# Kernel optimization log

Hardware: AMD Instinct MI355X
Metric: run time of the kernel (lower is better)

The kernel has to match this reference:

```python
import jax, jax.numpy as jnp
import numpy as np

INPUT_DIM = 1024
BOTTLENECK = 256
NUM_Q = 8
CODEBOOK = 1024
COMMIT_W = 0.25

def setup_inputs() -> dict:
    key = jax.random.key(0)
    ks = jax.random.split(key, 10)
    s_in = 1.0 / np.sqrt(INPUT_DIM)
    s_bn = 1.0 / np.sqrt(BOTTLENECK)
    return {
        'x': jax.random.normal(ks[0], (8, 2048, INPUT_DIM), jnp.float32),
        'W_e1': jax.random.uniform(ks[1], (INPUT_DIM, INPUT_DIM), jnp.float32, -s_in, s_in),
        'b_e1': jnp.zeros((INPUT_DIM,), jnp.float32),
        'W_e2': jax.random.uniform(ks[2], (INPUT_DIM, BOTTLENECK), jnp.float32, -s_in, s_in),
        'b_e2': jnp.zeros((BOTTLENECK,), jnp.float32),
        'codebooks': jax.random.normal(ks[3], (NUM_Q, CODEBOOK, BOTTLENECK), jnp.float32),
        'W_d1': jax.random.uniform(ks[4], (BOTTLENECK, INPUT_DIM), jnp.float32, -s_bn, s_bn),
        'b_d1': jnp.zeros((INPUT_DIM,), jnp.float32),
        'W_d2': jax.random.uniform(ks[5], (INPUT_DIM, INPUT_DIM), jnp.float32, -s_in, s_in),
        'b_d2': jnp.zeros((INPUT_DIM,), jnp.float32),
    }

def _gelu(x):
    return jax.nn.gelu(x, approximate=False)  # torch nn.GELU default = exact erf

def _rvq(z_flat, codebooks):
    # z_flat: [N, D]; codebooks: [Q, K, D]
    def step(res, cb):
        # squared L2 distances via expansion: [N, K]
        d2 = (jnp.sum(res * res, -1, keepdims=True)
              - 2.0 * res @ cb.T
              + jnp.sum(cb * cb, -1))
        idx = jnp.argmin(d2, axis=-1)                      # [N]
        q = jax.lax.stop_gradient(jnp.take(cb, idx, 0))    # [N, D] (EMA codebook: no grad)
        closs = jnp.mean((res - q) ** 2)
        return res - q, (idx, q, closs)
    _, (indices, qs, closses) = jax.lax.scan(step, z_flat, codebooks)
    q_total = jnp.sum(qs, axis=0)
    # straight-through estimator
    quantized = z_flat + jax.lax.stop_gradient(q_total - z_flat)
    commitment = COMMIT_W * jnp.mean(closses)
    return quantized, indices, commitment

def reference(x, W_e1, b_e1, W_e2, b_e2, codebooks, W_d1, b_d1, W_d2, b_d2):
    lead = x.shape[:-1]
    z = _gelu(x @ W_e1 + b_e1) @ W_e2 + b_e2               # [..., BOTTLENECK]
    zf = z.reshape(-1, BOTTLENECK)
    qf, indices, commitment = _rvq(zf, codebooks)
    quantized = qf.reshape(*lead, BOTTLENECK)
    indices = indices.reshape(NUM_Q, *lead)
    reconstructed = _gelu(quantized @ W_d1 + b_d1) @ W_d2 + b_d2
    return z, quantized, indices, reconstructed, commitment
```

## Files before the change

kernel.cpp:

```cpp
#include <hip/hip_runtime.h>
#include <math.h>

#define NROWS 16384
#define DIN   1024
#define DBN   256
#define NQ    8
#define NCODE 1024
#define MARGIN 2.0f

#define OFF_Z    0
#define OFF_Q    4194304
#define OFF_IDX  8388608
#define OFF_REC  8519680
#define OFF_COM  25296896

typedef __attribute__((ext_vector_type(8))) short short8v;
typedef __attribute__((ext_vector_type(4))) float f32x4;

__device__ __forceinline__ float gelu_f(float x) {
  return 0.5f * x * (1.0f + erff(x * 0.70710678118654752440f));
}

__device__ __forceinline__ ushort f2b(float x) {
  unsigned u = __float_as_uint(x);
  unsigned r = u + 0x7FFF + ((u >> 16) & 1);
  return (ushort)(r >> 16);
}
__device__ __forceinline__ float b2f(ushort u) {
  return __uint_as_float((unsigned)u << 16);
}
__device__ __forceinline__ void split3(float v, ushort& s1, ushort& s2, ushort& s3) {
  s1 = f2b(v);
  const float r1 = v - b2f(s1);
  s2 = f2b(r1);
  const float r2 = r1 - b2f(s2);
  s3 = f2b(r2);
}

template<bool GELU, int NB, int OUT>
__global__ __launch_bounds__(256) void gemm6(
    const float* __restrict__ Af,
    const ushort* __restrict__ B1, const ushort* __restrict__ B2,
    const ushort* __restrict__ B3,
    const float* __restrict__ bias,
    float* __restrict__ C0, float* __restrict__ C1,
    int N, int K)
{
  constexpr int BN = NB * 32;
  __shared__ char lds[24576 + BN * 192];
  char* ldsA = lds;
  char* ldsB = lds + 24576;
  const int tid = threadIdx.x;
  const int bm = blockIdx.x * 128;
  const int bn = blockIdx.y * BN;
  const int lane = tid & 63;
  const int wid = tid >> 6;
  const int wr = wid >> 1, wc = wid & 1;

  const int srow = tid >> 1, skh = tid & 1;
  const float* Ap = Af + (size_t)(bm + srow) * K + skh * 16;
  const int abase = srow * 192;
  const int aswz = (srow & 7) << 4;

  f32x4 acc[4][NB];
  #pragma unroll
  for (int m = 0; m < 4; ++m)
    #pragma unroll
    for (int n = 0; n < NB; ++n) acc[m][n] = (f32x4)0.f;

  union U8 { ushort u[8]; short8v v; };

  const int nt = K >> 5;
  for (int t = 0; t < nt; ++t) {
    const int k0 = t << 5;
    __syncthreads();
    float av[16];
    *(float4*)&av[0]  = *(const float4*)(Ap + k0);
    *(float4*)&av[4]  = *(const float4*)(Ap + k0 + 4);
    *(float4*)&av[8]  = *(const float4*)(Ap + k0 + 8);
    *(float4*)&av[12] = *(const float4*)(Ap + k0 + 12);
    U8 p1[2], p2[2], p3[2];
    #pragma unroll
    for (int i = 0; i < 16; ++i) {
      ushort s1, s2, s3;
      split3(av[i], s1, s2, s3);
      p1[i >> 3].u[i & 7] = s1;
      p2[i >> 3].u[i & 7] = s2;
      p3[i >> 3].u[i & 7] = s3;
    }
    #pragma unroll
    for (int h2 = 0; h2 < 2; ++h2) {
      const int kb = skh * 32 + h2 * 16;
      *(short8v*)(ldsA + ((abase + 0   + kb) ^ aswz)) = p1[h2].v;
      *(short8v*)(ldsA + ((abase + 64  + kb) ^ aswz)) = p2[h2].v;
      *(short8v*)(ldsA + ((abase + 128 + kb) ^ aswz)) = p3[h2].v;
    }
    if (NB == 4) {
      const int br = tid >> 1, bk = tid & 1;
      const size_t g = (size_t)(bn + br) * K + k0 + bk * 16;
      const int bb = br * 192, bswz = (br & 7) << 4;
      #pragma unroll
      for (int h2 = 0; h2 < 2; ++h2) {
        const int kb = bk * 32 + h2 * 16;
        *(uint4*)(ldsB + ((bb + 0   + kb) ^ bswz)) = *(const uint4*)(B1 + g + h2 * 8);
        *(uint4*)(ldsB + ((bb + 64  + kb) ^ bswz)) = *(const uint4*)(B2 + g + h2 * 8);
        *(uint4*)(ldsB + ((bb + 128 + kb) ^ bswz)) = *(const uint4*)(B3 + g + h2 * 8);
      }
    } else {
      const int br = tid >> 2, bk = tid & 3;
      const size_t g = (size_t)(bn + br) * K + k0 + bk * 8;
      const int bb = br * 192, bswz = (br & 7) << 4;
      const int kb = bk * 16;
      *(uint4*)(ldsB + ((bb + 0   + kb) ^ bswz)) = *(const uint4*)(B1 + g);
      *(uint4*)(ldsB + ((bb + 64  + kb) ^ bswz)) = *(const uint4*)(B2 + g);
      *(uint4*)(ldsB + ((bb + 128 + kb) ^ bswz)) = *(const uint4*)(B3 + g);
    }
    __syncthreads();

    const int kq = (lane >> 4) << 4;
    short8v a1[4], a2[4], a3[4], b1v[NB], b2v[NB], b3v[NB];
    #pragma unroll
    for (int m = 0; m < 4; ++m) {
      const int row = wr * 64 + m * 16 + (lane & 15);
      const int base = row * 192, swz = (row & 7) << 4;
      a1[m] = *(const short8v*)(ldsA + ((base + 0   + kq) ^ swz));
      a2[m] = *(const short8v*)(ldsA + ((base + 64  + kq) ^ swz));
      a3[m] = *(const short8v*)(ldsA + ((base + 128 + kq) ^ swz));
    }
    #pragma unroll
    for (int n = 0; n < NB; ++n) {
      const int row = wc * (NB * 16) + n * 16 + (lane & 15);
      const int base = row * 192, swz = (row & 7) << 4;
      b1v[n] = *(const short8v*)(ldsB + ((base + 0   + kq) ^ swz));
      b2v[n] = *(const short8v*)(ldsB + ((base + 64  + kq) ^ swz));
      b3v[n] = *(const short8v*)(ldsB + ((base + 128 + kq) ^ swz));
    }
    #pragma unroll
    for (int m = 0; m < 4; ++m)
      #pragma unroll
      for (int n = 0; n < NB; ++n) {
        f32x4 a = acc[m][n];
        a = __builtin_amdgcn_mfma_f32_16x16x32_bf16(a3[m], b1v[n], a, 0, 0, 0);
        a = __builtin_amdgcn_mfma_f32_16x16x32_bf16(a1[m], b3v[n], a, 0, 0, 0);
        a = __builtin_amdgcn_mfma_f32_16x16x32_bf16(a2[m], b2v[n], a, 0, 0, 0);
        a = __builtin_amdgcn_mfma_f32_16x16x32_bf16(a2[m], b1v[n], a, 0, 0, 0);
        a = __builtin_amdgcn_mfma_f32_16x16x32_bf16(a1[m], b2v[n], a, 0, 0, 0);
        a = __builtin_amdgcn_mfma_f32_16x16x32_bf16(a1[m], b1v[n], a, 0, 0, 0);
        acc[m][n] = a;
      }
  }

  #pragma unroll
  for (int n = 0; n < NB; ++n) {
    const int col = bn + wc * (NB * 16) + n * 16 + (lane & 15);
    const float bb = bias[col];
    #pragma unroll
    for (int m = 0; m < 4; ++m) {
      const int row0 = bm + wr * 64 + m * 16 + ((lane >> 4) << 2);
      #pragma unroll
      for (int r = 0; r < 4; ++r) {
        float v = acc[m][n][r] + bb;
        if (GELU) v = gelu_f(v);
        C0[(size_t)(row0 + r) * N + col] = v;
        if (OUT == 1) C1[(size_t)(row0 + r) * N + col] = v;
      }
    }
  }
}

__device__ __forceinline__ void mm_core(
    const ushort* __restrict__ A, const ushort* __restrict__ B,
    int K, int bm, int bn, char* lds, f32x4 acc[4][4])
{
  char* ldsA = lds;
  char* ldsB = lds + 16384;
  const int tid = threadIdx.x;
  const int lane = tid & 63;
  const int wid = tid >> 6;
  const int wr = wid >> 1, wc = wid & 1;

  #pragma unroll
  for (int m = 0; m < 4; ++m)
    #pragma unroll
    for (int n = 0; n < 4; ++n) acc[m][n] = (f32x4)0.f;

  const int nt = K >> 6;
  for (int t = 0; t < nt; ++t) {
    const int k0 = t << 6;
    __syncthreads();
    #pragma unroll
    for (int c = 0; c < 4; ++c) {
      const int id = c * 256 + tid;
      const int row = id >> 3, k8 = id & 7;
      const uint4 va = *(const uint4*)(A + (size_t)(bm + row) * K + k0 + k8 * 8);
      const uint4 vb = *(const uint4*)(B + (size_t)(bn + row) * K + k0 + k8 * 8);
      const int off = (row * 128 + k8 * 16) ^ ((row & 7) << 4);
      *(uint4*)(ldsA + off) = va;
      *(uint4*)(ldsB + off) = vb;
    }
    __syncthreads();
    #pragma unroll
    for (int kk = 0; kk < 2; ++kk) {
      short8v af[4], bfr[4];
      #pragma unroll
      for (int m = 0; m < 4; ++m) {
        const int row = wr * 64 + m * 16 + (lane & 15);
        af[m] = *(const short8v*)(ldsA +
            ((row * 128 + kk * 64 + ((lane >> 4) << 4)) ^ ((row & 7) << 4)));
      }
      #pragma unroll
      for (int n = 0; n < 4; ++n) {
        const int row = wc * 64 + n * 16 + (lane & 15);
        bfr[n] = *(const short8v*)(ldsB +
            ((row * 128 + kk * 64 + ((lane >> 4) << 4)) ^ ((row & 7) << 4)));
      }
      #pragma unroll
      for (int m = 0; m < 4; ++m)
        #pragma unroll
        for (int n = 0; n < 4; ++n)
          acc[m][n] = __builtin_amdgcn_mfma_f32_16x16x32_bf16(
              af[m], bfr[n], acc[m][n], 0, 0, 0);
    }
  }
}

__global__ __launch_bounds__(256) void rvq_screen(
    const ushort* __restrict__ resb, const ushort* __restrict__ cbb,
    const float* __restrict__ cnorm, _Float16* __restrict__ D)
{
  __shared__ char lds[32768];
  f32x4 acc[4][4];
  const int bm = blockIdx.x * 128, bn = blockIdx.y * 128;
  mm_core(resb, cbb, DBN, bm, bn, lds, acc);
  const int lane = threadIdx.x & 63;
  const int wid = threadIdx.x >> 6;
  const int wr = wid >> 1, wc = wid & 1;
  #pragma unroll
  for (int n = 0; n < 4; ++n) {
    const int col = bn + wc * 64 + n * 16 + (lane & 15);
    const float cn = cnorm[col];
    #pragma unroll
    for (int m = 0; m < 4; ++m) {
      const int row0 = bm + wr * 64 + m * 16 + ((lane >> 4) << 2);
      #pragma unroll
      for (int r = 0; r < 4; ++r)
        D[(size_t)(row0 + r) * NCODE + col] = (_Float16)(cn - 2.0f * acc[m][n][r]);
    }
  }
}

template<bool GELU, bool OUTF>
__global__ __launch_bounds__(256) void gemm_bf16(
    const ushort* __restrict__ A, const ushort* __restrict__ Bt,
    const float* __restrict__ bias, float* __restrict__ Cf,
    ushort* __restrict__ Cb, int N, int K)
{
  __shared__ char lds[32768];
  f32x4 acc[4][4];
  const int bm = blockIdx.x * 128, bn = blockIdx.y * 128;
  mm_core(A, Bt, K, bm, bn, lds, acc);
  const int lane = threadIdx.x & 63;
  const int wid = threadIdx.x >> 6;
  const int wr = wid >> 1, wc = wid & 1;
  #pragma unroll
  for (int n = 0; n < 4; ++n) {
    const int col = bn + wc * 64 + n * 16 + (lane & 15);
    const float bb = bias[col];
    #pragma unroll
    for (int m = 0; m < 4; ++m) {
      const int row0 = bm + wr * 64 + m * 16 + ((lane >> 4) << 2);
      #pragma unroll
      for (int r = 0; r < 4; ++r) {
        float v = acc[m][n][r] + bb;
        if (GELU) v = gelu_f(v);
        if (OUTF) Cf[(size_t)(row0 + r) * N + col] = v;
        else      Cb[(size_t)(row0 + r) * N + col] = f2b(v);
      }
    }
  }
}

__global__ __launch_bounds__(256) void cnorm_kernel(
    const float* __restrict__ cb, float* __restrict__ cnorm)
{
  const int code = blockIdx.x * 4 + (threadIdx.x >> 6);
  const int lane = threadIdx.x & 63;
  float4 v = *(const float4*)(cb + (size_t)code * DBN + lane * 4);
  float s = v.x * v.x + v.y * v.y + v.z * v.z + v.w * v.w;
  #pragma unroll
  for (int o = 32; o > 0; o >>= 1) s += __shfl_down(s, o, 64);
  if (lane == 0) cnorm[code] = s;
}

__global__ __launch_bounds__(256) void rvq_rescore(
    const _Float16* __restrict__ D, const float* __restrict__ cb_s,
    const float* __restrict__ cnorm_s,
    float* __restrict__ res, ushort* __restrict__ resb,
    float* __restrict__ idx_out, float* __restrict__ closs_part)
{
  __shared__ int cnt[4];
  __shared__ ushort cand[4][128];
  __shared__ float wsum[4];
  const int w = threadIdx.x >> 6, lane = threadIdx.x & 63;
  const int row = blockIdx.x * 4 + w;
  if (lane == 0) cnt[w] = 0;

  union H8 { uint4 u; _Float16 h[8]; };
  const _Float16* Dr = D + (size_t)row * NCODE + lane * 16;
  H8 a0, a1;
  a0.u = *(const uint4*)(Dr);
  a1.u = *(const uint4*)(Dr + 8);
  float dv[16];
  #pragma unroll
  for (int i = 0; i < 8; ++i) { dv[i] = (float)a0.h[i]; dv[8 + i] = (float)a1.h[i]; }

  float mn = dv[0];
  #pragma unroll
  for (int i = 1; i < 16; ++i) mn = fminf(mn, dv[i]);
  #pragma unroll
  for (int o = 32; o > 0; o >>= 1) mn = fminf(mn, __shfl_xor(mn, o, 64));
  const float thr = mn + MARGIN;

  #pragma unroll
  for (int i = 0; i < 16; ++i)
    if (dv[i] < thr) {
      int p = atomicAdd(&cnt[w], 1);
      if (p < 128) cand[w][p] = (ushort)(lane * 16 + i);
    }
  const int ncand = min(cnt[w], 128);

  const float4 r4 = *(const float4*)(res + (size_t)row * DBN + lane * 4);
  float bestv = INFINITY; int besti = 0x7fffffff;
  for (int c = 0; c < ncand; ++c) {
    const int code = cand[w][c];
    const float4 c4 = *(const float4*)(cb_s + (size_t)code * DBN + lane * 4);
    float d = r4.x * c4.x + r4.y * c4.y + r4.z * c4.z + r4.w * c4.w;
    #pragma unroll
    for (int o = 32; o > 0; o >>= 1) d += __shfl_xor(d, o, 64);
    const float ex = cnorm_s[code] - 2.0f * d;
    if (ex < bestv || (ex == bestv && code < besti)) { bestv = ex; besti = code; }
  }

  const float4 q4 = *(const float4*)(cb_s + (size_t)besti * DBN + lane * 4);
  float4 n4;
  n4.x = r4.x - q4.x; n4.y = r4.y - q4.y; n4.z = r4.z - q4.z; n4.w = r4.w - q4.w;
  *(float4*)(res + (size_t)row * DBN + lane * 4) = n4;
  ushort4 nb;
  nb.x = f2b(n4.x); nb.y = f2b(n4.y); nb.z = f2b(n4.z); nb.w = f2b(n4.w);
  *(ushort4*)(resb + (size_t)row * DBN + lane * 4) = nb;

  float s = n4.x * n4.x + n4.y * n4.y + n4.z * n4.z + n4.w * n4.w;
  #pragma unroll
  for (int o = 32; o > 0; o >>= 1) s += __shfl_xor(s, o, 64);
  if (lane == 0) { wsum[w] = s; idx_out[row] = (float)besti; }
  __syncthreads();
  if (threadIdx.x == 0)
    closs_part[blockIdx.x] = wsum[0] + wsum[1] + wsum[2] + wsum[3];
}

__global__ __launch_bounds__(256) void qfix_gather(
    const float* __restrict__ z, const float* __restrict__ idxf,
    const float* __restrict__ cb, float* __restrict__ q, ushort* __restrict__ qb)
{
  const int w = threadIdx.x >> 6, lane = threadIdx.x & 63;
  const int row = blockIdx.x * 4 + w;
  float4 a; a.x = 0.f; a.y = 0.f; a.z = 0.f; a.w = 0.f;
  #pragma unroll
  for (int s = 0; s < NQ; ++s) {
    const int ix = (int)idxf[(size_t)s * NROWS + row];
    const float4 c4 = *(const float4*)(cb + ((size_t)s * NCODE + ix) * DBN + lane * 4);
    a.x += c4.x; a.y += c4.y; a.z += c4.z; a.w += c4.w;
  }
  const float4 z4 = *(const float4*)(z + (size_t)row * DBN + lane * 4);
  float4 qv;
  qv.x = z4.x + (a.x - z4.x); qv.y = z4.y + (a.y - z4.y);
  qv.z = z4.z + (a.z - z4.z); qv.w = z4.w + (a.w - z4.w);
  *(float4*)(q + (size_t)row * DBN + lane * 4) = qv;
  ushort4 qb4;
  qb4.x = f2b(qv.x); qb4.y = f2b(qv.y); qb4.z = f2b(qv.z); qb4.w = f2b(qv.w);
  *(ushort4*)(qb + (size_t)row * DBN + lane * 4) = qb4;
}

__global__ __launch_bounds__(256) void conv_flat(
    const float* __restrict__ in, ushort* __restrict__ out, int n4)
{
  const int i = blockIdx.x * 256 + threadIdx.x;
  if (i >= n4) return;
  const float4 v = *(const float4*)(in + (size_t)i * 4);
  ushort4 o;
  o.x = f2b(v.x); o.y = f2b(v.y); o.z = f2b(v.z); o.w = f2b(v.w);
  *(ushort4*)(out + (size_t)i * 4) = o;
}

__global__ __launch_bounds__(256) void convT(
    const float* __restrict__ in, ushort* __restrict__ out, int K, int N)
{
  __shared__ float t[32][33];
  const int k0 = blockIdx.x * 32, n0 = blockIdx.y * 32;
  const int tx = threadIdx.x & 31, ty = threadIdx.x >> 5;
  #pragma unroll
  for (int i = 0; i < 32; i += 8)
    t[ty + i][tx] = in[(size_t)(k0 + ty + i) * N + n0 + tx];
  __syncthreads();
  #pragma unroll
  for (int i = 0; i < 32; i += 8)
    out[(size_t)(n0 + ty + i) * K + k0 + tx] = f2b(t[tx][ty + i]);
}

__global__ __launch_bounds__(256) void convT_split3(
    const float* __restrict__ in, ushort* __restrict__ o1,
    ushort* __restrict__ o2, ushort* __restrict__ o3, int K, int N)
{
  __shared__ float t[32][33];
  const int k0 = blockIdx.x * 32, n0 = blockIdx.y * 32;
  const int tx = threadIdx.x & 31, ty = threadIdx.x >> 5;
  #pragma unroll
  for (int i = 0; i < 32; i += 8)
    t[ty + i][tx] = in[(size_t)(k0 + ty + i) * N + n0 + tx];
  __syncthreads();
  #pragma unroll
  for (int i = 0; i < 32; i += 8) {
    const float v = t[tx][ty + i];
    ushort s1, s2, s3;
    split3(v, s1, s2, s3);
    const size_t o = (size_t)(n0 + ty + i) * K + k0 + tx;
    o1[o] = s1; o2[o] = s2; o3[o] = s3;
  }
}

__global__ __launch_bounds__(256) void commit_kernel(
    const float* __restrict__ parts, float* __restrict__ out)
{
  __shared__ float sm[256];
  float s = 0.f;
  for (int i = threadIdx.x; i < NQ * 4096; i += 256) s += parts[i];
  sm[threadIdx.x] = s;
  __syncthreads();
  for (int st = 128; st > 0; st >>= 1) {
    if (threadIdx.x < st) sm[threadIdx.x] += sm[threadIdx.x + st];
    __syncthreads();
  }
  if (threadIdx.x == 0)
    out[0] = 0.25f * sm[0] / (8.0f * 4194304.0f);
}

extern "C" void kernel_launch(void* const* d_in, const int* in_sizes, int n_in,
                              void* d_out, int out_size, void* d_ws, size_t ws_size,
                              hipStream_t stream) {
  (void)in_sizes; (void)n_in; (void)out_size; (void)ws_size;
  const float* x    = (const float*)d_in[0];
  const float* W_e1 = (const float*)d_in[1];
  const float* b_e1 = (const float*)d_in[2];
  const float* W_e2 = (const float*)d_in[3];
  const float* b_e2 = (const float*)d_in[4];
  const float* cb   = (const float*)d_in[5];
  const float* W_d1 = (const float*)d_in[6];
  const float* b_d1 = (const float*)d_in[7];
  const float* W_d2 = (const float*)d_in[8];
  const float* b_d2 = (const float*)d_in[9];

  float* out = (float*)d_out;
  float* z_out   = out + OFF_Z;
  float* q_out   = out + OFF_Q;
  float* idx_out = out + OFF_IDX;
  float* rec_out = out + OFF_REC;
  float* com_out = out + OFF_COM;

  float* ws      = (float*)d_ws;
  float* hidden  = ws;
  float* res     = ws + 16777216;
  float* cnorm   = ws + 20971520;
  float* closs   = ws + 20979712;
  ushort* wtail  = (ushort*)(ws + 21012480);
  ushort* We2T1  = wtail;
  ushort* We2T2  = wtail + 262144;
  ushort* We2T3  = wtail + 524288;
  ushort* Wd1T   = wtail + 786432;
  ushort* Wd2T   = wtail + 1048576;

  ushort* resu   = (ushort*)res;
  ushort* We1T1  = resu;
  ushort* We1T2  = resu + 1048576;
  ushort* We1T3  = resu + 2097152;

  ushort* hregion = (ushort*)d_ws;
  _Float16* Dmat = (_Float16*)hregion;
  ushort* resb   = hregion + 16777216;
  ushort* cbb    = hregion + 20971520;
  ushort* qb     = hregion + 20971520;
  ushort* hidb   = hregion;

  cnorm_kernel<<<2048, 256, 0, stream>>>(cb, cnorm);
  convT_split3<<<dim3(32, 32), 256, 0, stream>>>(W_e1, We1T1, We1T2, We1T3, DIN, DIN);
  convT_split3<<<dim3(32, 8),  256, 0, stream>>>(W_e2, We2T1, We2T2, We2T3, DIN, DBN);
  convT<<<dim3(8, 32),  256, 0, stream>>>(W_d1, Wd1T, DBN, DIN);
  convT<<<dim3(32, 32), 256, 0, stream>>>(W_d2, Wd2T, DIN, DIN);

  gemm6<true,  4, 0><<<dim3(128, 8), 256, 0, stream>>>(
      x, We1T1, We1T2, We1T3, b_e1, hidden, nullptr, DIN, DIN);
  gemm6<false, 2, 1><<<dim3(128, 4), 256, 0, stream>>>(
      hidden, We2T1, We2T2, We2T3, b_e2, z_out, res, DBN, DIN);

  conv_flat<<<4096, 256, 0, stream>>>(res, resb, 1048576);
  conv_flat<<<2048, 256, 0, stream>>>(cb, cbb, 524288);

  for (int s = 0; s < NQ; ++s) {
    rvq_screen<<<dim3(128, 8), 256, 0, stream>>>(
        resb, cbb + (size_t)s * NCODE * DBN, cnorm + s * NCODE, Dmat);
    rvq_rescore<<<4096, 256, 0, stream>>>(
        Dmat, cb + (size_t)s * NCODE * DBN, cnorm + s * NCODE,
        res, resb, idx_out + (size_t)s * NROWS, closs + s * 4096);
  }

  qfix_gather<<<4096, 256, 0, stream>>>(z_out, idx_out, cb, q_out, qb);

  gemm_bf16<true,  false><<<dim3(128, 8), 256, 0, stream>>>(qb, Wd1T, b_d1, nullptr, hidb, DIN, DBN);
  gemm_bf16<false, true ><<<dim3(128, 8), 256, 0, stream>>>(hidb, Wd2T, b_d2, rec_out, nullptr, DIN, DIN);

  commit_kernel<<<1, 256, 0, stream>>>(closs, com_out);
}
```

Baseline: 682.1 us.

## Replace dense fp16 RVQ distance matrix with compact per-tile candidate records

```diff
diff --git a/kernel.cpp b/kernel.cpp
--- a/kernel.cpp
+++ b/kernel.cpp
@@ -226,26 +226,79 @@
 
 __global__ __launch_bounds__(256) void rvq_screen(
     const ushort* __restrict__ resb, const ushort* __restrict__ cbb,
-    const float* __restrict__ cnorm, _Float16* __restrict__ D)
+    const float* __restrict__ cnorm, uint4* __restrict__ Srec)
 {
   __shared__ char lds[32768];
   f32x4 acc[4][4];
   const int bm = blockIdx.x * 128, bn = blockIdx.y * 128;
   mm_core(resb, cbb, DBN, bm, bn, lds, acc);
-  const int lane = threadIdx.x & 63;
-  const int wid = threadIdx.x >> 6;
+  __syncthreads();
+
+  float* rv    = (float*)lds;
+  float* cminA = (float*)(lds + 16384);
+  int*   scnt  = (int*)(lds + 16896);
+  uint*  scand = (uint*)(lds + 17408);
+
+  const int tid = threadIdx.x;
+  const int lane = tid & 63;
+  const int wid = tid >> 6;
   const int wr = wid >> 1, wc = wid & 1;
-  #pragma unroll
-  for (int n = 0; n < 4; ++n) {
-    const int col = bn + wc * 64 + n * 16 + (lane & 15);
-    const float cn = cnorm[col];
-    #pragma unroll
-    for (int m = 0; m < 4; ++m) {
-      const int row0 = bm + wr * 64 + m * 16 + ((lane >> 4) << 2);
-      #pragma unroll
-      for (int r = 0; r < 4; ++r)
-        D[(size_t)(row0 + r) * NCODE + col] = (_Float16)(cn - 2.0f * acc[m][n][r]);
-    }
+  const int l15 = lane & 15, lq = lane >> 4;
+
+  float cn[4];
+  #pragma unroll
+  for (int n = 0; n < 4; ++n) cn[n] = cnorm[bn + wc * 64 + n * 16 + l15];
+
+  #pragma unroll
+  for (int m = 0; m < 4; ++m)
+    #pragma unroll
+    for (int r = 0; r < 4; ++r) {
+      const int row = wr * 64 + m * 16 + lq * 4 + r;
+      float mn = cn[0] - 2.0f * acc[m][0][r];
+      #pragma unroll
+      for (int n = 1; n < 4; ++n)
+        mn = fminf(mn, cn[n] - 2.0f * acc[m][n][r]);
+      rv[row * 32 + wc * 16 + l15] = mn;
+    }
+  __syncthreads();
+  if (tid < 128) {
+    float c = rv[tid * 32];
+    #pragma unroll
+    for (int i = 1; i < 32; ++i) c = fminf(c, rv[tid * 32 + i]);
+    cminA[tid] = c;
+    scnt[tid] = 0;
+  }
+  __syncthreads();
+  #pragma unroll
+  for (int m = 0; m < 4; ++m)
+    #pragma unroll
+    for (int n = 0; n < 4; ++n)
+      #pragma unroll
+      for (int r = 0; r < 4; ++r) {
+        const int row = wr * 64 + m * 16 + lq * 4 + r;
+        const float d2 = cn[n] - 2.0f * acc[m][n][r];
+        if (d2 <= cminA[row] + MARGIN) {
+          const int p = atomicAdd(&scnt[row], 1);
+          if (p < 12) {
+            union { _Float16 h; ushort u; } cv;
+            cv.h = (_Float16)d2;
+            const uint col = (uint)(bn + wc * 64 + n * 16 + l15);
+            scand[row * 12 + p] = (col << 16) | (uint)cv.u;
+          }
+        }
+      }
+  __syncthreads();
+  if (tid < 128) {
+    uint s[12];
+    #pragma unroll
+    for (int i = 0; i < 12; ++i) s[i] = scand[tid * 12 + i];
+    uint4 w0, w1, w2, w3;
+    w0.x = __float_as_uint(cminA[tid]); w0.y = (uint)scnt[tid]; w0.z = s[0]; w0.w = s[1];
+    w1.x = s[2]; w1.y = s[3]; w1.z = s[4]; w1.w = s[5];
+    w2.x = s[6]; w2.y = s[7]; w2.z = s[8]; w2.w = s[9];
+    w3.x = s[10]; w3.y = s[11]; w3.z = 0u; w3.w = 0u;
+    uint4* p = Srec + ((size_t)blockIdx.y * NROWS + bm + tid) * 4;
+    p[0] = w0; p[1] = w1; p[2] = w2; p[3] = w3;
   }
 }
 
@@ -293,41 +346,53 @@
 }
 
 __global__ __launch_bounds__(256) void rvq_rescore(
-    const _Float16* __restrict__ D, const float* __restrict__ cb_s,
+    const uint4* __restrict__ Srec, const float* __restrict__ cb_s,
     const float* __restrict__ cnorm_s,
     float* __restrict__ res, ushort* __restrict__ resb,
     float* __restrict__ idx_out, float* __restrict__ closs_part)
 {
-  __shared__ int cnt[4];
-  __shared__ ushort cand[4][128];
+  __shared__ int cnt4[4];
+  __shared__ ushort cand[4][1024];
   __shared__ float wsum[4];
   const int w = threadIdx.x >> 6, lane = threadIdx.x & 63;
   const int row = blockIdx.x * 4 + w;
-  if (lane == 0) cnt[w] = 0;
-
-  union H8 { uint4 u; _Float16 h[8]; };
-  const _Float16* Dr = D + (size_t)row * NCODE + lane * 16;
-  H8 a0, a1;
-  a0.u = *(const uint4*)(Dr);
-  a1.u = *(const uint4*)(Dr + 8);
-  float dv[16];
-  #pragma unroll
-  for (int i = 0; i < 8; ++i) { dv[i] = (float)a0.h[i]; dv[8 + i] = (float)a1.h[i]; }
-
-  float mn = dv[0];
-  #pragma unroll
-  for (int i = 1; i < 16; ++i) mn = fminf(mn, dv[i]);
-  #pragma unroll
-  for (int o = 32; o > 0; o >>= 1) mn = fminf(mn, __shfl_xor(mn, o, 64));
-  const float thr = mn + MARGIN;
-
-  #pragma unroll
-  for (int i = 0; i < 16; ++i)
-    if (dv[i] < thr) {
-      int p = atomicAdd(&cnt[w], 1);
-      if (p < 128) cand[w][p] = (ushort)(lane * 16 + i);
-    }
-  const int ncand = min(cnt[w], 128);
+  if (lane == 0) cnt4[w] = 0;
+
+  float minv = INFINITY;
+  uint rcnt = 0;
+  uint4 r0, r1, r2, r3;
+  if (lane < 8) {
+    const uint4* p = Srec + ((size_t)lane * NROWS + row) * 4;
+    r0 = p[0]; r1 = p[1]; r2 = p[2]; r3 = p[3];
+    minv = __uint_as_float(r0.x);
+    rcnt = r0.y;
+  }
+  float g = minv;
+  #pragma unroll
+  for (int o = 32; o > 0; o >>= 1) g = fminf(g, __shfl_xor(g, o, 64));
+  const float thr = g + MARGIN;
+
+  if (lane < 8) {
+    if (rcnt <= 12) {
+      uint s[12] = { r0.z, r0.w, r1.x, r1.y, r1.z, r1.w,
+                     r2.x, r2.y, r2.z, r2.w, r3.x, r3.y };
+      for (uint i = 0; i < rcnt; ++i) {
+        union { ushort u; _Float16 h; } cv;
+        cv.u = (ushort)(s[i] & 0xFFFFu);
+        if ((float)cv.h <= thr) {
+          const int p = atomicAdd(&cnt4[w], 1);
+          if (p < 1024) cand[w][p] = (ushort)(s[i] >> 16);
+        }
+      }
+    } else {
+      for (int c = 0; c < 128; ++c) {
+        const int p = atomicAdd(&cnt4[w], 1);
+        if (p < 1024) cand[w][p] = (ushort)(lane * 128 + c);
+      }
+    }
+  }
+  __syncthreads();
+  const int ncand = min(cnt4[w], 1024);
 
   const float4 r4 = *(const float4*)(res + (size_t)row * DBN + lane * 4);
   float bestv = INFINITY; int besti = 0x7fffffff;
@@ -484,7 +549,7 @@
   ushort* We1T3  = resu + 2097152;
 
   ushort* hregion = (ushort*)d_ws;
-  _Float16* Dmat = (_Float16*)hregion;
+  uint4*  Srec   = (uint4*)hregion;
   ushort* resb   = hregion + 16777216;
   ushort* cbb    = hregion + 20971520;
   ushort* qb     = hregion + 20971520;
@@ -506,9 +571,9 @@
 
   for (int s = 0; s < NQ; ++s) {
     rvq_screen<<<dim3(128, 8), 256, 0, stream>>>(
-        resb, cbb + (size_t)s * NCODE * DBN, cnorm + s * NCODE, Dmat);
+        resb, cbb + (size_t)s * NCODE * DBN, cnorm + s * NCODE, Srec);
     rvq_rescore<<<4096, 256, 0, stream>>>(
-        Dmat, cb + (size_t)s * NCODE * DBN, cnorm + s * NCODE,
+        Srec, cb + (size_t)s * NCODE * DBN, cnorm + s * NCODE,
         res, resb, idx_out + (size_t)s * NROWS, closs + s * 4096);
   }
 
```

Result: no change. 694.3 us (median of 2 runs) (+1.8%).
